# Optimization experiments

Measured on AMD Instinct MI355X. Metric: run time of the kernel, lower is better.

## Reference

```python
import jax, jax.numpy as jnp
import numpy as np

NC = 128        # num_clusters
WSZ = 64        # window_size (query and kv window)
NMEM = 1        # num_mem_kv
COMMITMENT = 1e-4
EPS = 1e-5      # scatter_mean eps


def _l2norm(x):
    # matches torch F.normalize(p=2, dim=-1, eps=1e-12)
    n = jnp.linalg.norm(x, axis=-1, keepdims=True)
    return x / jnp.maximum(n, 1e-12)


def setup_inputs() -> dict:
    key = jax.random.key(0)
    ks = jax.random.split(key, 6)
    b, h, t, d = 4, 8, 8192, 64
    q = jax.random.normal(ks[0], (b, h, t, d), jnp.float32)
    k = jax.random.normal(ks[1], (b, h, t, d), jnp.float32)
    v = jax.random.normal(ks[2], (b, h, t, d), jnp.float32)
    means = jax.random.normal(ks[3], (h, NC, d), jnp.float32)
    mem_key = jax.random.normal(ks[4], (h, NC, NMEM, d), jnp.float32)
    mem_value = jax.random.normal(ks[5], (h, NC, NMEM, d), jnp.float32)
    return {"q": q, "k": k, "v": v, "means": means,
            "mem_key": mem_key, "mem_value": mem_value}


def reference(q, k, v, means, mem_key, mem_value):
    b, h, t, d = q.shape
    scale = d ** -0.5

    # ---- Kmeans.forward (eval: initted, no means update) ----
    x = _l2norm(jnp.concatenate([q, k], axis=2))              # [b,h,2t,d]
    dists = jnp.einsum('bhld,hcd->bhlc', x, means)            # [b,h,2t,nc]
    buckets = jnp.argmax(dists, axis=-1)                      # [b,h,2t]
    means_b = jnp.broadcast_to(means[None], (b,) + means.shape)
    routed = jnp.take_along_axis(means_b, buckets[..., None], axis=2)  # [b,h,2t,d]
    aux_loss = jnp.mean((x - routed) ** 2) * COMMITMENT

    q_dists, k_dists = dists[:, :, :t], dists[:, :, t:]

    # ---- distribution(): top-wsz tokens per cluster ----
    def route(ds, w):
        # ds [b,h,L,nc] -> indices [b,h,nc*w]; top_k over token axis per cluster
        _, idx = jax.lax.top_k(jnp.swapaxes(ds, -1, -2), w)   # [b,h,nc,w]
        return idx.reshape(b, h, -1)

    indices = route(q_dists, WSZ)                             # [b,h,nc*wsz]
    kv_indices = route(k_dists, WSZ)

    gather = lambda vals, idx: jnp.take_along_axis(vals, idx[..., None], axis=2)
    qg = gather(q, indices).reshape(b, h, NC, WSZ, d)
    kg = gather(k, kv_indices).reshape(b, h, NC, WSZ, d)
    vg = gather(v, kv_indices).reshape(b, h, NC, WSZ, d)

    # prepend mem kv per cluster
    mk = jnp.broadcast_to(mem_key[None], (b,) + mem_key.shape)   # [b,h,nc,nmem,d]
    mv = jnp.broadcast_to(mem_value[None], (b,) + mem_value.shape)
    kg = jnp.concatenate([mk, kg], axis=3)                    # [b,h,nc,nmem+wsz,d]
    vg = jnp.concatenate([mv, vg], axis=3)

    dots = jnp.einsum('bhnid,bhnjd->bhnij', qg, kg) * scale
    attn = jax.nn.softmax(dots, axis=-1)
    bo = jnp.einsum('bhnij,bhnjd->bhnid', attn, vg)
    so = bo.reshape(b, h, NC * WSZ, d)

    # ---- scatter_mean back to [b,h,t,d] ----
    def scat(src, idx):  # src [t',d], idx [t']
        num = jnp.zeros((t, d), src.dtype).at[idx].add(src)
        den = jnp.zeros((t, d), src.dtype).at[idx].add(jnp.ones_like(src))
        return num / (den + EPS)

    out = jax.vmap(jax.vmap(scat))(so, indices)
    return out, aux_loss
```

## Files before the change

### kernel.cpp

```cpp
#include <hip/hip_runtime.h>
#include <math.h>
#include <stdint.h>

#define B_   4
#define H_   8
#define BH   32
#define T_   8192
#define D_   64
#define NC_  128
#define WSZ_ 64
#define CAND_CAP 512

typedef unsigned short u16;
typedef _Float16 frag8h __attribute__((ext_vector_type(8)));
typedef float floatx4 __attribute__((ext_vector_type(4)));

__device__ inline unsigned pack2h(float a, float b) {
    union { _Float16 h[2]; unsigned u; } p;
    p.h[0] = (_Float16)a; p.h[1] = (_Float16)b;
    return p.u;
}

__global__ __launch_bounds__(256) void means16_kernel(
    const float* __restrict__ means, u16* __restrict__ means16, float* __restrict__ msq)
{
    int i = (blockIdx.x * 256 + threadIdx.x) * 4;
    float4 mv = *(const float4*)(means + i);
    uint2 pk = { pack2h(mv.x, mv.y), pack2h(mv.z, mv.w) };
    *(uint2*)&means16[i] = pk;
    float s = mv.x*mv.x + mv.y*mv.y + mv.z*mv.z + mv.w*mv.w;
    s += __shfl_xor(s, 1); s += __shfl_xor(s, 2);
    s += __shfl_xor(s, 4); s += __shfl_xor(s, 8);
    if ((threadIdx.x & 15) == 0) msq[i >> 6] = s;
}

__global__ __launch_bounds__(256, 5) void dist_kernel(
    const float* __restrict__ qg, const float* __restrict__ kg,
    const u16* __restrict__ means16, const float* __restrict__ msq,
    u16* __restrict__ dbuf,
    double* __restrict__ rnorm, double* __restrict__ aux_sum, int pair0)
{
    __shared__ u16 s_ov[128 * 68];
    __shared__ float s_aux;
    const int tid = threadIdx.x;
    const int bh = pair0 + blockIdx.y;
    const int h  = bh & 7;
    const int tok0 = blockIdx.x * 64;
    const int isK  = (tok0 >= T_) ? 1 : 0;
    const int tloc0 = isK ? tok0 - T_ : tok0;
    const float* src = isK ? kg : qg;

    if (tid == 0) s_aux = 0.f;
    const int row = tid >> 2, sub = tid & 3;
    {
        float xr[16];
        const float* sp = src + ((size_t)bh * T_ + tloc0 + row) * D_ + sub * 16;
        #pragma unroll
        for (int e4 = 0; e4 < 4; e4++) {
            float4 xv = *(const float4*)(sp + e4 * 4);
            xr[e4*4+0] = xv.x; xr[e4*4+1] = xv.y; xr[e4*4+2] = xv.z; xr[e4*4+3] = xv.w;
        }
        double dss = 0.0;
        #pragma unroll
        for (int e = 0; e < 16; e++) { double dv = (double)xr[e]; dss += dv * dv; }
        dss += __shfl_xor(dss, 1); dss += __shfl_xor(dss, 2);
        if (sub == 0) {
            double rn64 = 1.0 / fmax(sqrt(dss), 1e-12);
            rnorm[((size_t)bh * 2 + isK) * T_ + tloc0 + row] = rn64;
        }
        float ss = (float)dss;
        const float rn = 1.0f / fmaxf(sqrtf(ss), 1e-12f);
        #pragma unroll
        for (int e = 0; e < 16; e++) xr[e] *= rn;
        uint4 p0 = { pack2h(xr[0],xr[1]), pack2h(xr[2],xr[3]), pack2h(xr[4],xr[5]), pack2h(xr[6],xr[7]) };
        uint4 p1 = { pack2h(xr[8],xr[9]), pack2h(xr[10],xr[11]), pack2h(xr[12],xr[13]), pack2h(xr[14],xr[15]) };
        *(uint4*)&s_ov[row * 72 + sub * 16]     = p0;
        *(uint4*)&s_ov[row * 72 + sub * 16 + 8] = p1;
    }
    const int w = tid >> 6, lane = tid & 63;
    const int mrow = lane & 15, quad = lane >> 4;
    frag8h b0[8], b1[8];
    {
        const u16* mb = means16 + (size_t)h * (NC_ * D_);
        #pragma unroll
        for (int n = 0; n < 8; n++) {
            b0[n] = *(const frag8h*)&mb[(n*16 + mrow)*64 + quad*8];
            b1[n] = *(const frag8h*)&mb[(n*16 + mrow)*64 + 32 + quad*8];
        }
    }
    __syncthreads();
    const frag8h a0 = *(const frag8h*)&s_ov[(w*16 + mrow)*72 + quad*8];
    const frag8h a1 = *(const frag8h*)&s_ov[(w*16 + mrow)*72 + 32 + quad*8];
    __syncthreads();
    {
        float bv[4]; int bc[4];
        #pragma unroll
        for (int r = 0; r < 4; r++) { bv[r] = -1e30f; bc[r] = 0; }
        const int tokw = w * 16 + quad * 4;
        #pragma unroll
        for (int n = 0; n < 8; n++) {
            floatx4 acc = {0.f, 0.f, 0.f, 0.f};
            acc = __builtin_amdgcn_mfma_f32_16x16x32_f16(a0, b0[n], acc, 0, 0, 0);
            acc = __builtin_amdgcn_mfma_f32_16x16x32_f16(a1, b1[n], acc, 0, 0, 0);
            const int cc = n*16 + mrow;
            uint2 pk = { pack2h(acc[0], acc[1]), pack2h(acc[2], acc[3]) };
            *(uint2*)&s_ov[cc * 68 + tokw] = pk;
            #pragma unroll
            for (int r = 0; r < 4; r++)
                if (acc[r] > bv[r]) { bv[r] = acc[r]; bc[r] = cc; }
        }
        #pragma unroll
        for (int m = 1; m < 16; m <<= 1) {
            #pragma unroll
            for (int r = 0; r < 4; r++) {
                float ov = __shfl_xor(bv[r], m);
                int   oc = __shfl_xor(bc[r], m);
                if (ov > bv[r] || (ov == bv[r] && oc < bc[r])) { bv[r] = ov; bc[r] = oc; }
            }
        }
        if (mrow == 0) {
            const float* mq = msq + (h << 7);
            float rs = 0.f;
            #pragma unroll
            for (int r = 0; r < 4; r++) rs += 1.0f - 2.0f * bv[r] + mq[bc[r]];
            atomicAdd(&s_aux, rs);
        }
    }
    __syncthreads();
    {
        const size_t dbase = ((size_t)blockIdx.y*2 + isK) * NC_;
        #pragma unroll
        for (int it = 0; it < 8; it++) {
            int idx = it * 256 + tid;
            int crow = idx >> 4;
            int colg = (idx & 15) * 4;
            uint2 pk = *(const uint2*)&s_ov[crow * 68 + colg];
            *(uint2*)&dbuf[(dbase + crow) * T_ + tloc0 + colg] = pk;
        }
    }
    if (tid == 0) atomicAdd(aux_sum, (double)s_aux);
}

__global__ __launch_bounds__(256) void topk_kernel(
    const u16* __restrict__ dbuf, const float* __restrict__ qg,
    const float* __restrict__ kg, const float* __restrict__ means,
    const double* __restrict__ rnorm,
    int* __restrict__ idx_q, int* __restrict__ idx_k, int pair0)
{
    __shared__ int s_hist[2048];
    __shared__ int s_scan[256];
    __shared__ int s_wtot[4];
    __shared__ int s_B, s_cnt;
    __shared__ int s_cand[CAND_CAP];
    __shared__ unsigned long long s_key[CAND_CAP];
    __shared__ int s_tok[CAND_CAP];
    __shared__ double s_mean[64];

    const int tid = threadIdx.x;
    const int lane = tid & 63, w = tid >> 6;
    const int c = blockIdx.x, isK = blockIdx.y, pl = blockIdx.z;
    const int bh = pair0 + pl, h = bh & 7;
    const u16* row = dbuf + (((size_t)pl*2 + isK)*NC_ + c)*T_;

    for (int i = tid; i < 2048; i += 256) s_hist[i] = 0;
    if (tid < 64) s_mean[tid] = (double)means[((size_t)h*NC_ + c)*D_ + tid];
    __syncthreads();
    u16 keys[32];
    {
        const uint4* rv = (const uint4*)(row + tid * 32);
        #pragma unroll
        for (int j4 = 0; j4 < 4; j4++) {
            uint4 pk = rv[j4];
            unsigned int wd[4] = {pk.x, pk.y, pk.z, pk.w};
            #pragma unroll
            for (int w2 = 0; w2 < 4; w2++) {
                u16 lo = (u16)(wd[w2] & 0xffffu), hi = (u16)(wd[w2] >> 16);
                keys[j4*8 + w2*2 + 0] = (lo & 0x8000u) ? (u16)(~lo) : (u16)(lo | 0x8000u);
                keys[j4*8 + w2*2 + 1] = (hi & 0x8000u) ? (u16)(~hi) : (u16)(hi | 0x8000u);
            }
        }
    }
    #pragma unroll
    for (int j = 0; j < 32; j++) {
        int b = keys[j] >> 4;
        atomicAdd(&s_hist[b >> 1], 1 << ((b & 1) * 16));
    }
    __syncthreads();
    int cs = 0;
    #pragma unroll
    for (int k2 = 0; k2 < 8; k2++) { int v2 = s_hist[tid*8 + k2]; cs += (v2 & 0xffff) + (v2 >> 16); }
    int sv = cs;
    #pragma unroll
    for (int off = 1; off < 64; off <<= 1) {
        int o = __shfl_down(sv, off);
        if (lane + off < 64) sv += o;
    }
    if (lane == 0) s_wtot[w] = sv;
    __syncthreads();
    {
        int add = 0;
        #pragma unroll
        for (int w2 = 0; w2 < 4; w2++) if (w2 > w) add += s_wtot[w2];
        s_scan[tid] = sv + add;
    }
    __syncthreads();
    {
        int Tj = s_scan[tid];
        int Tn = (tid < 255) ? s_scan[tid + 1] : 0;
        if (Tj >= WSZ_ && Tn < WSZ_) {
            int running = Tn, Bb = tid * 16;
            for (int b2 = tid*16 + 15; b2 >= tid*16; b2--) {
                running += (s_hist[b2 >> 1] >> ((b2 & 1) * 16)) & 0xffff;
                if (running >= WSZ_) { Bb = b2; break; }
            }
            s_B = Bb;
        }
    }
    __syncthreads();
    int thr = s_B - 2; if (thr < 0) thr = 0;
    for (;;) {
        if (tid == 0) s_cnt = 0;
        __syncthreads();
        #pragma unroll
        for (int j = 0; j < 32; j++) {
            if ((int)(keys[j] >> 4) >= thr) {
                int p = atomicAdd(&s_cnt, 1);
                if (p < CAND_CAP) s_cand[p] = tid*32 + j;
            }
        }
        __syncthreads();
        if (s_cnt <= CAND_CAP) break;
        thr++;
        __syncthreads();
    }
    const int M = s_cnt;
    const float* src = isK ? kg : qg;
    const double* rnrow = rnorm + ((size_t)bh * 2 + isK) * T_;
    {
        const int sub = tid & 3;
        for (int ci = (tid >> 2); ci < M; ci += 64) {
            const int tok = s_cand[ci];
            const float* xr = src + ((size_t)bh*T_ + tok)*D_ + sub*16;
            double dot = 0.0;
            #pragma unroll
            for (int e4 = 0; e4 < 4; e4++) {
                float4 xv4 = *(const float4*)(xr + e4*4);
                const double* mm = &s_mean[sub*16 + e4*4];
                dot += (double)xv4.x*mm[0] + (double)xv4.y*mm[1]
                     + (double)xv4.z*mm[2] + (double)xv4.w*mm[3];
            }
            dot += __shfl_xor(dot, 1); dot += __shfl_xor(dot, 2);
            if (sub == 0) {
                double val = dot * rnrow[tok];
                unsigned long long u = (unsigned long long)__double_as_longlong(val);
                u = (u & 0x8000000000000000ull) ? ~u : (u | 0x8000000000000000ull);
                s_key[ci] = u;
                s_tok[ci] = tok;
            }
        }
    }
    __syncthreads();
    int* dst = (isK ? idx_k : idx_q) + ((size_t)bh*NC_ + c)*WSZ_;
    for (int p = tid; p < M; p += 256) {
        unsigned long long kp = s_key[p];
        int ip = s_tok[p];
        int rank = 0;
        for (int j = 0; j < M; j++) {
            unsigned long long kj = s_key[j];
            int ij = s_tok[j];
            if (kj > kp || (kj == kp && ij < ip)) rank++;
        }
        if (rank < WSZ_) dst[rank] = ip;
    }
}

__global__ __launch_bounds__(256) void count_kernel(
    const int* __restrict__ idx_q, int* __restrict__ counts)
{
    int i = blockIdx.x * 256 + threadIdx.x;
    int bh = i >> 13;
    atomicAdd(&counts[bh * T_ + idx_q[i]], 1);
}

__global__ __launch_bounds__(256) void scan_kernel(
    const int* __restrict__ counts, int* __restrict__ offsets, int* __restrict__ cursor)
{
    __shared__ int s_tmp[256];
    const int tid = threadIdx.x, bh = blockIdx.x;
    const int base = bh * T_;
    int c[32], s = 0;
    #pragma unroll
    for (int j = 0; j < 32; j++) { c[j] = counts[base + tid*32 + j]; s += c[j]; }
    s_tmp[tid] = s;
    __syncthreads();
    for (int off = 1; off < 256; off <<= 1) {
        int add = (tid >= off) ? s_tmp[tid - off] : 0;
        __syncthreads();
        s_tmp[tid] += add;
        __syncthreads();
    }
    int running = s_tmp[tid] - s + bh * (NC_ * WSZ_);
    #pragma unroll
    for (int j = 0; j < 32; j++) {
        offsets[base + tid*32 + j] = running;
        cursor [base + tid*32 + j] = running;
        running += c[j];
    }
}

__global__ __launch_bounds__(256) void fill_kernel(
    const int* __restrict__ idx_q, int* __restrict__ cursor, u16* __restrict__ entries)
{
    int i = blockIdx.x * 256 + threadIdx.x;
    int bh = i >> 13;
    int tok = idx_q[i];
    int pos = atomicAdd(&cursor[bh * T_ + tok], 1);
    entries[pos] = (u16)(i & 8191);
}

__global__ __launch_bounds__(256) void attn_kernel(
    const float* __restrict__ qg, const float* __restrict__ kg, const float* __restrict__ vg,
    const float* __restrict__ mem_k, const float* __restrict__ mem_v,
    const int* __restrict__ idx_q, const int* __restrict__ idx_k,
    float* __restrict__ bo)
{
    __shared__ u16 s_k[80 * 72];
    __shared__ u16 s_vt[64 * 72];
    __shared__ int s_qi[WSZ_], s_ki[WSZ_];
    const int tid = threadIdx.x;
    const int c = blockIdx.x, bh = blockIdx.y, h = bh & 7;
    const int lane = tid & 63, w = tid >> 6;
    const int mrow = lane & 15, quad = lane >> 4;

    if (tid < WSZ_) {
        s_qi[tid] = idx_q[((size_t)bh*NC_ + c)*WSZ_ + tid];
        s_ki[tid] = idx_k[((size_t)bh*NC_ + c)*WSZ_ + tid];
    }
    __syncthreads();

    frag8h a0, a1;
    {
        const int qtok = s_qi[w*16 + mrow];
        const float* qr = qg + ((size_t)bh*T_ + qtok)*D_ + quad*8;
        float4 x0 = *(const float4*)(qr);
        float4 x1 = *(const float4*)(qr + 4);
        float4 x2 = *(const float4*)(qr + 32);
        float4 x3 = *(const float4*)(qr + 36);
        a0 = (frag8h){ (_Float16)x0.x,(_Float16)x0.y,(_Float16)x0.z,(_Float16)x0.w,
                       (_Float16)x1.x,(_Float16)x1.y,(_Float16)x1.z,(_Float16)x1.w };
        a1 = (frag8h){ (_Float16)x2.x,(_Float16)x2.y,(_Float16)x2.z,(_Float16)x2.w,
                       (_Float16)x3.x,(_Float16)x3.y,(_Float16)x3.z,(_Float16)x3.w };
    }

    for (int i = tid; i < 320; i += 256) {
        const int r = i >> 2, sub = i & 3;
        if (r < 65) {
            const float* kp; const float* vp;
            if (r == 0) {
                kp = mem_k + ((size_t)h*NC_ + c)*D_ + sub*16;
                vp = mem_v + ((size_t)h*NC_ + c)*D_ + sub*16;
            } else {
                const int tok = s_ki[r-1];
                kp = kg + ((size_t)bh*T_ + tok)*D_ + sub*16;
                vp = vg + ((size_t)bh*T_ + tok)*D_ + sub*16;
            }
            float kv4[16], vv4[16];
            #pragma unroll
            for (int e4 = 0; e4 < 4; e4++) {
                float4 a = *(const float4*)(kp + e4*4);
                float4 b = *(const float4*)(vp + e4*4);
                kv4[e4*4+0]=a.x; kv4[e4*4+1]=a.y; kv4[e4*4+2]=a.z; kv4[e4*4+3]=a.w;
                vv4[e4*4+0]=b.x; vv4[e4*4+1]=b.y; vv4[e4*4+2]=b.z; vv4[e4*4+3]=b.w;
            }
            uint4 pk0 = { pack2h(kv4[0],kv4[1]),  pack2h(kv4[2],kv4[3]),
                          pack2h(kv4[4],kv4[5]),  pack2h(kv4[6],kv4[7]) };
            uint4 pk1 = { pack2h(kv4[8],kv4[9]),  pack2h(kv4[10],kv4[11]),
                          pack2h(kv4[12],kv4[13]),pack2h(kv4[14],kv4[15]) };
            *(uint4*)&s_k[r*72 + sub*16]     = pk0;
            *(uint4*)&s_k[r*72 + sub*16 + 8] = pk1;
            #pragma unroll
            for (int e = 0; e < 16; e++)
                *(_Float16*)&s_vt[(sub*16 + e)*72 + r] = (_Float16)vv4[e];
        } else {
            uint4 z = {0,0,0,0};
            *(uint4*)&s_k[r*72 + sub*16]     = z;
            *(uint4*)&s_k[r*72 + sub*16 + 8] = z;
        }
    }
    __syncthreads();

    floatx4 S[5];
    #pragma unroll
    for (int t = 0; t < 5; t++) {
        const frag8h b0 = *(const frag8h*)&s_k[(t*16 + mrow)*72 + quad*8];
        const frag8h b1 = *(const frag8h*)&s_k[(t*16 + mrow)*72 + 32 + quad*8];
        floatx4 acc = {0.f,0.f,0.f,0.f};
        acc = __builtin_amdgcn_mfma_f32_16x16x32_f16(a0, b0, acc, 0, 0, 0);
        acc = __builtin_amdgcn_mfma_f32_16x16x32_f16(a1, b1, acc, 0, 0, 0);
        S[t] = acc;
    }
    __syncthreads();

    if (mrow != 0) { S[4][0]=-1e30f; S[4][1]=-1e30f; S[4][2]=-1e30f; S[4][3]=-1e30f; }

    float l[4];
    u16* sp = s_k + w * 1152;
    #pragma unroll
    for (int r = 0; r < 4; r++) {
        float m = fmaxf(fmaxf(fmaxf(S[0][r], S[1][r]), fmaxf(S[2][r], S[3][r])), S[4][r]);
        #pragma unroll
        for (int msk = 1; msk < 16; msk <<= 1) m = fmaxf(m, __shfl_xor(m, msk));
        float p16v[5];
        float ps = 0.f;
        #pragma unroll
        for (int t = 0; t < 5; t++) {
            float p = __expf((S[t][r] - m) * 0.125f);
            p16v[t] = (float)(_Float16)p;
            ps += p16v[t];
        }
        #pragma unroll
        for (int msk = 1; msk < 16; msk <<= 1) ps += __shfl_xor(ps, msk);
        l[r] = ps;
        #pragma unroll
        for (int t = 0; t < 4; t++)
            *(_Float16*)&sp[(quad*4 + r)*72 + t*16 + mrow] = (_Float16)p16v[t];
        S[4][r] = p16v[4];
    }

    const frag8h pa0 = *(const frag8h*)&sp[mrow*72 + quad*8];
    const frag8h pa1 = *(const frag8h*)&sp[mrow*72 + 32 + quad*8];
    float pm[4];
    #pragma unroll
    for (int r = 0; r < 4; r++) pm[r] = __shfl(S[4][r], lane & 48);
    floatx4 O[4];
    #pragma unroll
    for (int dt = 0; dt < 4; dt++) {
        const frag8h vb0 = *(const frag8h*)&s_vt[(dt*16 + mrow)*72 + quad*8];
        const frag8h vb1 = *(const frag8h*)&s_vt[(dt*16 + mrow)*72 + 32 + quad*8];
        floatx4 acc = {0.f,0.f,0.f,0.f};
        acc = __builtin_amdgcn_mfma_f32_16x16x32_f16(pa0, vb0, acc, 0, 0, 0);
        acc = __builtin_amdgcn_mfma_f32_16x16x32_f16(pa1, vb1, acc, 0, 0, 0);
        const float v64 = (float)*(const _Float16*)&s_vt[(dt*16 + mrow)*72 + 64];
        #pragma unroll
        for (int r = 0; r < 4; r++) acc[r] += pm[r] * v64;
        O[dt] = acc;
    }

    #pragma unroll
    for (int r = 0; r < 4; r++) {
        const float rl = 1.f / l[r];
        float* orow = bo + (((size_t)bh*NC_ + c)*WSZ_ + w*16 + quad*4 + r)*D_ + mrow;
        #pragma unroll
        for (int dt = 0; dt < 4; dt++)
            orow[dt*16] = O[dt][r] * rl;
    }
}

__global__ __launch_bounds__(256) void gather_kernel(
    const float* __restrict__ bo, const u16* __restrict__ entries,
    const int* __restrict__ offsets, const int* __restrict__ counts,
    const double* __restrict__ aux_sum, float* __restrict__ out)
{
    const int tid = threadIdx.x;
    const int g = blockIdx.x * 4 + (tid >> 6);
    const int lane = tid & 63;
    const int bh = g >> 13;
    const int start = offsets[g];
    const int len = counts[g];
    float sum = 0.f;
    for (int e = 0; e < len; e++) {
        int ent = entries[start + e];
        sum += bo[(((size_t)bh << 13) | (unsigned)ent) * D_ + lane];
    }
    out[(size_t)g * D_ + lane] = sum / ((float)len + 1e-5f);
    if (blockIdx.x == 0 && tid == 0)
        out[(size_t)BH * T_ * D_] = (float)(aux_sum[0] * (0.0001 / 33554432.0));
}

extern "C" void kernel_launch(void* const* d_in, const int* in_sizes, int n_in,
                              void* d_out, int out_size, void* d_ws, size_t ws_size,
                              hipStream_t stream)
{
    const float* q      = (const float*)d_in[0];
    const float* k      = (const float*)d_in[1];
    const float* v      = (const float*)d_in[2];
    const float* means  = (const float*)d_in[3];
    const float* mem_k  = (const float*)d_in[4];
    const float* mem_v  = (const float*)d_in[5];
    float* out = (float*)d_out;

    char* ws = (char*)d_ws;
    const size_t SZ_TOK = (size_t)BH * T_ * sizeof(int);
    const size_t SZ_IDX = (size_t)BH * NC_ * WSZ_ * sizeof(int);
    size_t off = 256;
    const size_t o_counts  = off; off += SZ_TOK;
    const size_t o_offsets = off; off += SZ_TOK;
    const size_t o_cursor  = off; off += SZ_TOK;
    const size_t o_entries = off; off += (size_t)BH * NC_ * WSZ_ * sizeof(u16);
    const size_t o_idxq    = off; off += SZ_IDX;
    const size_t o_idxk    = off; off += SZ_IDX;
    const size_t o_rnorm   = off; off += (size_t)BH * 2 * T_ * sizeof(double);
    const size_t o_m16     = off; off += (size_t)H_ * NC_ * D_ * sizeof(u16);
    const size_t o_msq     = off; off += (size_t)H_ * NC_ * sizeof(float);
    size_t o_bo = (off + 255) & ~(size_t)255;
    off = o_bo + (size_t)BH * NC_ * WSZ_ * D_ * sizeof(float);
    size_t o_dbuf = (off + 255) & ~(size_t)255;

    double* aux   = (double*)ws;
    int* counts   = (int*)(ws + o_counts);
    int* offsets  = (int*)(ws + o_offsets);
    int* cursor   = (int*)(ws + o_cursor);
    u16* entries  = (u16*)(ws + o_entries);
    int* idxq     = (int*)(ws + o_idxq);
    int* idxk     = (int*)(ws + o_idxk);
    double* rnorm = (double*)(ws + o_rnorm);
    u16* m16      = (u16*)(ws + o_m16);
    float* msq    = (float*)(ws + o_msq);
    float* bo     = (float*)(ws + o_bo);
    u16* dbuf     = (u16*)(ws + o_dbuf);

    const size_t per_pair = (size_t)2 * NC_ * T_ * sizeof(u16);
    int CH = 32;
    while (CH > 1 && o_dbuf + (size_t)CH * per_pair > ws_size) CH >>= 1;

    hipMemsetAsync(ws, 0, o_offsets, stream);
    means16_kernel<<<dim3(H_ * NC_ * D_ / 1024), 256, 0, stream>>>(means, m16, msq);

    for (int p0 = 0; p0 < BH; p0 += CH) {
        dim3 gA(256, CH);
        dist_kernel<<<gA, 256, 0, stream>>>(q, k, m16, msq, dbuf, rnorm, aux, p0);
        dim3 gB(NC_, 2, CH);
        topk_kernel<<<gB, 256, 0, stream>>>(dbuf, q, k, means, rnorm, idxq, idxk, p0);
    }
    count_kernel<<<dim3(BH * NC_ * WSZ_ / 256), 256, 0, stream>>>(idxq, counts);
    scan_kernel<<<dim3(BH), 256, 0, stream>>>(counts, offsets, cursor);
    fill_kernel<<<dim3(BH * NC_ * WSZ_ / 256), 256, 0, stream>>>(idxq, cursor, entries);
    attn_kernel<<<dim3(NC_, BH), 256, 0, stream>>>(q, k, v, mem_k, mem_v, idxq, idxk, bo);
    gather_kernel<<<dim3(BH * T_ / 4), 256, 0, stream>>>(bo, entries, offsets, counts, aux, out);
}
```

Measured before the change: 496.0 us.

## Quantize distance buffer to 8-bit and shard aux-loss atomics

```diff
diff --git a/kernel.cpp b/kernel.cpp
--- a/kernel.cpp
+++ b/kernel.cpp
@@ -12,6 +12,7 @@
 #define CAND_CAP 512
 
 typedef unsigned short u16;
+typedef unsigned char u8;
 typedef _Float16 frag8h __attribute__((ext_vector_type(8)));
 typedef float floatx4 __attribute__((ext_vector_type(4)));
 
@@ -22,7 +23,8 @@
 }
 
 __global__ __launch_bounds__(256) void means16_kernel(
-    const float* __restrict__ means, u16* __restrict__ means16, float* __restrict__ msq)
+    const float* __restrict__ means, u16* __restrict__ means16,
+    float* __restrict__ msq, float* __restrict__ mscale)
 {
     int i = (blockIdx.x * 256 + threadIdx.x) * 4;
     float4 mv = *(const float4*)(means + i);
@@ -31,16 +33,21 @@
     float s = mv.x*mv.x + mv.y*mv.y + mv.z*mv.z + mv.w*mv.w;
     s += __shfl_xor(s, 1); s += __shfl_xor(s, 2);
     s += __shfl_xor(s, 4); s += __shfl_xor(s, 8);
-    if ((threadIdx.x & 15) == 0) msq[i >> 6] = s;
-}
-
-__global__ __launch_bounds__(256, 5) void dist_kernel(
+    if ((threadIdx.x & 15) == 0) {
+        msq[i >> 6] = s;
+        mscale[i >> 6] = 127.5f / fmaxf(sqrtf(s), 1e-6f);
+    }
+}
+
+__global__ __launch_bounds__(256, 6) void dist_kernel(
     const float* __restrict__ qg, const float* __restrict__ kg,
     const u16* __restrict__ means16, const float* __restrict__ msq,
-    u16* __restrict__ dbuf,
-    double* __restrict__ rnorm, double* __restrict__ aux_sum, int pair0)
-{
-    __shared__ u16 s_ov[128 * 68];
+    const float* __restrict__ mscale,
+    u8* __restrict__ dbuf,
+    double* __restrict__ rnorm, double* __restrict__ aux_arr, int pair0)
+{
+    __shared__ u16 s_xb[64 * 72];
+    __shared__ float s_sc[128];
     __shared__ float s_aux;
     const int tid = threadIdx.x;
     const int bh = pair0 + blockIdx.y;
@@ -51,6 +58,7 @@
     const float* src = isK ? kg : qg;
 
     if (tid == 0) s_aux = 0.f;
+    if (tid < 128) s_sc[tid] = mscale[(h << 7) + tid];
     const int row = tid >> 2, sub = tid & 3;
     {
         float xr[16];
@@ -74,8 +82,8 @@
         for (int e = 0; e < 16; e++) xr[e] *= rn;
         uint4 p0 = { pack2h(xr[0],xr[1]), pack2h(xr[2],xr[3]), pack2h(xr[4],xr[5]), pack2h(xr[6],xr[7]) };
         uint4 p1 = { pack2h(xr[8],xr[9]), pack2h(xr[10],xr[11]), pack2h(xr[12],xr[13]), pack2h(xr[14],xr[15]) };
-        *(uint4*)&s_ov[row * 72 + sub * 16]     = p0;
-        *(uint4*)&s_ov[row * 72 + sub * 16 + 8] = p1;
+        *(uint4*)&s_xb[row * 72 + sub * 16]     = p0;
+        *(uint4*)&s_xb[row * 72 + sub * 16 + 8] = p1;
     }
     const int w = tid >> 6, lane = tid & 63;
     const int mrow = lane & 15, quad = lane >> 4;
@@ -89,9 +97,10 @@
         }
     }
     __syncthreads();
-    const frag8h a0 = *(const frag8h*)&s_ov[(w*16 + mrow)*72 + quad*8];
-    const frag8h a1 = *(const frag8h*)&s_ov[(w*16 + mrow)*72 + 32 + quad*8];
-    __syncthreads();
+    const frag8h a0 = *(const frag8h*)&s_xb[(w*16 + mrow)*72 + quad*8];
+    const frag8h a1 = *(const frag8h*)&s_xb[(w*16 + mrow)*72 + 32 + quad*8];
+    __syncthreads();
+    u8* st = (u8*)s_xb;
     {
         float bv[4]; int bc[4];
         #pragma unroll
@@ -103,8 +112,12 @@
             acc = __builtin_amdgcn_mfma_f32_16x16x32_f16(a0, b0[n], acc, 0, 0, 0);
             acc = __builtin_amdgcn_mfma_f32_16x16x32_f16(a1, b1[n], acc, 0, 0, 0);
             const int cc = n*16 + mrow;
-            uint2 pk = { pack2h(acc[0], acc[1]), pack2h(acc[2], acc[3]) };
-            *(uint2*)&s_ov[cc * 68 + tokw] = pk;
+            const float sc = s_sc[cc];
+            unsigned q0 = (unsigned)(int)fminf(fmaxf(fmaf(acc[0], sc, 127.5f), 0.f), 255.f);
+            unsigned q1 = (unsigned)(int)fminf(fmaxf(fmaf(acc[1], sc, 127.5f), 0.f), 255.f);
+            unsigned q2 = (unsigned)(int)fminf(fmaxf(fmaf(acc[2], sc, 127.5f), 0.f), 255.f);
+            unsigned q3 = (unsigned)(int)fminf(fmaxf(fmaf(acc[3], sc, 127.5f), 0.f), 255.f);
+            *(unsigned*)&st[cc * 68 + tokw] = q0 | (q1 << 8) | (q2 << 16) | (q3 << 24);
             #pragma unroll
             for (int r = 0; r < 4; r++)
                 if (acc[r] > bv[r]) { bv[r] = acc[r]; bc[r] = cc; }
@@ -134,22 +147,21 @@
             int idx = it * 256 + tid;
             int crow = idx >> 4;
             int colg = (idx & 15) * 4;
-            uint2 pk = *(const uint2*)&s_ov[crow * 68 + colg];
-            *(uint2*)&dbuf[(dbase + crow) * T_ + tloc0 + colg] = pk;
-        }
-    }
-    if (tid == 0) atomicAdd(aux_sum, (double)s_aux);
+            unsigned pk = *(const unsigned*)&st[crow * 68 + colg];
+            *(unsigned*)&dbuf[(dbase + crow) * T_ + tloc0 + colg] = pk;
+        }
+    }
+    if (tid == 0) atomicAdd(&aux_arr[(blockIdx.x ^ blockIdx.y) & 63], (double)s_aux);
 }
 
 __global__ __launch_bounds__(256) void topk_kernel(
-    const u16* __restrict__ dbuf, const float* __restrict__ qg,
+    const u8* __restrict__ dbuf, const float* __restrict__ qg,
     const float* __restrict__ kg, const float* __restrict__ means,
     const double* __restrict__ rnorm,
     int* __restrict__ idx_q, int* __restrict__ idx_k, int pair0)
 {
-    __shared__ int s_hist[2048];
+    __shared__ int s_hist[128];
     __shared__ int s_scan[256];
-    __shared__ int s_wtot[4];
     __shared__ int s_B, s_cnt;
     __shared__ int s_cand[CAND_CAP];
     __shared__ unsigned long long s_key[CAND_CAP];
@@ -157,64 +169,41 @@
     __shared__ double s_mean[64];
 
     const int tid = threadIdx.x;
-    const int lane = tid & 63, w = tid >> 6;
     const int c = blockIdx.x, isK = blockIdx.y, pl = blockIdx.z;
     const int bh = pair0 + pl, h = bh & 7;
-    const u16* row = dbuf + (((size_t)pl*2 + isK)*NC_ + c)*T_;
-
-    for (int i = tid; i < 2048; i += 256) s_hist[i] = 0;
+    const u8* row = dbuf + (((size_t)pl*2 + isK)*NC_ + c)*T_;
+
+    if (tid < 128) s_hist[tid] = 0;
     if (tid < 64) s_mean[tid] = (double)means[((size_t)h*NC_ + c)*D_ + tid];
     __syncthreads();
-    u16 keys[32];
+    unsigned wd[8];
     {
         const uint4* rv = (const uint4*)(row + tid * 32);
-        #pragma unroll
-        for (int j4 = 0; j4 < 4; j4++) {
-            uint4 pk = rv[j4];
-            unsigned int wd[4] = {pk.x, pk.y, pk.z, pk.w};
-            #pragma unroll
-            for (int w2 = 0; w2 < 4; w2++) {
-                u16 lo = (u16)(wd[w2] & 0xffffu), hi = (u16)(wd[w2] >> 16);
-                keys[j4*8 + w2*2 + 0] = (lo & 0x8000u) ? (u16)(~lo) : (u16)(lo | 0x8000u);
-                keys[j4*8 + w2*2 + 1] = (hi & 0x8000u) ? (u16)(~hi) : (u16)(hi | 0x8000u);
-            }
-        }
+        uint4 a = rv[0], b = rv[1];
+        wd[0]=a.x; wd[1]=a.y; wd[2]=a.z; wd[3]=a.w;
+        wd[4]=b.x; wd[5]=b.y; wd[6]=b.z; wd[7]=b.w;
     }
     #pragma unroll
     for (int j = 0; j < 32; j++) {
-        int b = keys[j] >> 4;
+        int b = (wd[j >> 2] >> ((j & 3) * 8)) & 0xff;
         atomicAdd(&s_hist[b >> 1], 1 << ((b & 1) * 16));
     }
     __syncthreads();
-    int cs = 0;
-    #pragma unroll
-    for (int k2 = 0; k2 < 8; k2++) { int v2 = s_hist[tid*8 + k2]; cs += (v2 & 0xffff) + (v2 >> 16); }
-    int sv = cs;
-    #pragma unroll
-    for (int off = 1; off < 64; off <<= 1) {
-        int o = __shfl_down(sv, off);
-        if (lane + off < 64) sv += o;
-    }
-    if (lane == 0) s_wtot[w] = sv;
-    __syncthreads();
-    {
-        int add = 0;
-        #pragma unroll
-        for (int w2 = 0; w2 < 4; w2++) if (w2 > w) add += s_wtot[w2];
-        s_scan[tid] = sv + add;
-    }
-    __syncthreads();
-    {
-        int Tj = s_scan[tid];
-        int Tn = (tid < 255) ? s_scan[tid + 1] : 0;
-        if (Tj >= WSZ_ && Tn < WSZ_) {
-            int running = Tn, Bb = tid * 16;
-            for (int b2 = tid*16 + 15; b2 >= tid*16; b2--) {
-                running += (s_hist[b2 >> 1] >> ((b2 & 1) * 16)) & 0xffff;
-                if (running >= WSZ_) { Bb = b2; break; }
-            }
-            s_B = Bb;
-        }
+    {
+        int rb = 255 - tid;
+        s_scan[tid] = (s_hist[rb >> 1] >> ((rb & 1) * 16)) & 0xffff;
+    }
+    __syncthreads();
+    for (int off = 1; off < 256; off <<= 1) {
+        int add = (tid >= off) ? s_scan[tid - off] : 0;
+        __syncthreads();
+        s_scan[tid] += add;
+        __syncthreads();
+    }
+    {
+        int Sb  = s_scan[255 - tid];
+        int Sb1 = (tid < 255) ? s_scan[254 - tid] : 0;
+        if (Sb >= WSZ_ && Sb1 < WSZ_) s_B = tid;
     }
     __syncthreads();
     int thr = s_B - 2; if (thr < 0) thr = 0;
@@ -223,7 +212,8 @@
         __syncthreads();
         #pragma unroll
         for (int j = 0; j < 32; j++) {
-            if ((int)(keys[j] >> 4) >= thr) {
+            int bv = (wd[j >> 2] >> ((j & 3) * 8)) & 0xff;
+            if (bv >= thr) {
                 int p = atomicAdd(&s_cnt, 1);
                 if (p < CAND_CAP) s_cand[p] = tid*32 + j;
             }
@@ -459,7 +449,7 @@
 __global__ __launch_bounds__(256) void gather_kernel(
     const float* __restrict__ bo, const u16* __restrict__ entries,
     const int* __restrict__ offsets, const int* __restrict__ counts,
-    const double* __restrict__ aux_sum, float* __restrict__ out)
+    const double* __restrict__ aux_arr, float* __restrict__ out)
 {
     const int tid = threadIdx.x;
     const int g = blockIdx.x * 4 + (tid >> 6);
@@ -473,8 +463,13 @@
         sum += bo[(((size_t)bh << 13) | (unsigned)ent) * D_ + lane];
     }
     out[(size_t)g * D_ + lane] = sum / ((float)len + 1e-5f);
-    if (blockIdx.x == 0 && tid == 0)
-        out[(size_t)BH * T_ * D_] = (float)(aux_sum[0] * (0.0001 / 33554432.0));
+    if (blockIdx.x == 0 && tid < 64) {
+        double v = aux_arr[tid];
+        #pragma unroll
+        for (int m = 1; m < 64; m <<= 1) v += __shfl_xor(v, m);
+        if (tid == 0)
+            out[(size_t)BH * T_ * D_] = (float)(v * (0.0001 / 33554432.0));
+    }
 }
 
 extern "C" void kernel_launch(void* const* d_in, const int* in_sizes, int n_in,
@@ -492,7 +487,7 @@
     char* ws = (char*)d_ws;
     const size_t SZ_TOK = (size_t)BH * T_ * sizeof(int);
     const size_t SZ_IDX = (size_t)BH * NC_ * WSZ_ * sizeof(int);
-    size_t off = 256;
+    size_t off = 512;
     const size_t o_counts  = off; off += SZ_TOK;
     const size_t o_offsets = off; off += SZ_TOK;
     const size_t o_cursor  = off; off += SZ_TOK;
@@ -502,6 +497,7 @@
     const size_t o_rnorm   = off; off += (size_t)BH * 2 * T_ * sizeof(double);
     const size_t o_m16     = off; off += (size_t)H_ * NC_ * D_ * sizeof(u16);
     const size_t o_msq     = off; off += (size_t)H_ * NC_ * sizeof(float);
+    const size_t o_mscale  = off; off += (size_t)H_ * NC_ * sizeof(float);
     size_t o_bo = (off + 255) & ~(size_t)255;
     off = o_bo + (size_t)BH * NC_ * WSZ_ * D_ * sizeof(float);
     size_t o_dbuf = (off + 255) & ~(size_t)255;
@@ -516,19 +512,20 @@
     double* rnorm = (double*)(ws + o_rnorm);
     u16* m16      = (u16*)(ws + o_m16);
     float* msq    = (float*)(ws + o_msq);
+    float* mscale = (float*)(ws + o_mscale);
     float* bo     = (float*)(ws + o_bo);
-    u16* dbuf     = (u16*)(ws + o_dbuf);
-
-    const size_t per_pair = (size_t)2 * NC_ * T_ * sizeof(u16);
+    u8* dbuf      = (u8*)(ws + o_dbuf);
+
+    const size_t per_pair = (size_t)2 * NC_ * T_ * sizeof(u8);
     int CH = 32;
     while (CH > 1 && o_dbuf + (size_t)CH * per_pair > ws_size) CH >>= 1;
 
     hipMemsetAsync(ws, 0, o_offsets, stream);
-    means16_kernel<<<dim3(H_ * NC_ * D_ / 1024), 256, 0, stream>>>(means, m16, msq);
+    means16_kernel<<<dim3(H_ * NC_ * D_ / 1024), 256, 0, stream>>>(means, m16, msq, mscale);
 
     for (int p0 = 0; p0 < BH; p0 += CH) {
         dim3 gA(256, CH);
-        dist_kernel<<<gA, 256, 0, stream>>>(q, k, m16, msq, dbuf, rnorm, aux, p0);
+        dist_kernel<<<gA, 256, 0, stream>>>(q, k, m16, msq, mscale, dbuf, rnorm, aux, p0);
         dim3 gB(NC_, 2, CH);
         topk_kernel<<<gB, 256, 0, stream>>>(dbuf, q, k, means, rnorm, idxq, idxk, p0);
     }
```

Result: faster. 474.9 us (-4.2%).
